# Optimization experiments

Measured on AMD Instinct MI355X. Metric: run time of the kernel, lower is better.

The kernel has to match this reference:

```python
import jax, jax.numpy as jnp
import numpy as np

DIM = 1024
HDS = 16
HEAD_DIM = DIM // HDS
ISC = True


def setup_inputs() -> dict:
    key = jax.random.key(0)
    k = jax.random.split(key, 5)
    x = jax.random.normal(k[0], (4, 2048, DIM), dtype=jnp.float32)
    # Linear(dim, 3*dim): weight [3*dim, dim] (torch layout), bias [3*dim]
    scale = 1.0 / np.sqrt(DIM)
    w_qkv = jax.random.uniform(k[1], (3 * DIM, DIM), jnp.float32, -scale, scale)
    b_qkv = jax.random.uniform(k[2], (3 * DIM,), jnp.float32, -scale, scale)
    w_out = jax.random.uniform(k[3], (DIM, DIM), jnp.float32, -scale, scale)
    b_out = jax.random.uniform(k[4], (DIM,), jnp.float32, -scale, scale)
    return {"x": x, "w_qkv": w_qkv, "b_qkv": b_qkv, "w_out": w_out, "b_out": b_out}


def reference(x, w_qkv, b_qkv, w_out, b_out):
    b, s, dim = x.shape
    # QKV projection: x @ w_qkv.T + b_qkv -> split into q, k, v
    qkv = jnp.einsum('bsd,ed->bse', x, w_qkv) + b_qkv
    q, k, v = jnp.split(qkv, 3, axis=-1)
    # [b, s, dim] -> [b, h, s, hd]
    def to_heads(t):
        return t.reshape(b, s, HDS, HEAD_DIM).transpose(0, 2, 1, 3)
    q, k, v = to_heads(q), to_heads(k), to_heads(v)
    att = jnp.einsum('bhqd,bhkd->bhqk', q, k) * (HEAD_DIM ** -0.5)
    if ISC:
        mask = jnp.triu(jnp.ones((s, s), dtype=bool), k=1)  # True above diagonal
        att = jnp.where(mask[None, None], -jnp.inf, att)
    att = jax.nn.softmax(att, axis=-1)
    # dropout is identity in eval mode
    out = jnp.einsum('bhqk,bhkd->bhqd', att, v)
    out = out.transpose(0, 2, 1, 3).reshape(b, s, dim)
    out = jnp.einsum('bsd,ed->bse', out, w_out) + b_out
    return out
```

## Files before the change

kernel.cpp:

```cpp
#include <hip/hip_runtime.h>
#include <stdint.h>

typedef __bf16 bf16x8 __attribute__((ext_vector_type(8)));
typedef short s16x8 __attribute__((ext_vector_type(8)));
typedef short s16x4 __attribute__((ext_vector_type(4)));
typedef float f32x4 __attribute__((ext_vector_type(4)));
typedef unsigned short u16;

#define K_DIM 1024

static __device__ __forceinline__ u16 f2bf(float f) {
    uint32_t x = __float_as_uint(f);
    x += 0x7fffu + ((x >> 16) & 1u);
    return (u16)(x >> 16);
}

static __device__ __forceinline__ f32x4 mfma16(s16x8 a, s16x8 b, f32x4 c) {
    return __builtin_amdgcn_mfma_f32_16x16x32_bf16(
        __builtin_bit_cast(bf16x8, a), __builtin_bit_cast(bf16x8, b), c, 0, 0, 0);
}

static __device__ __forceinline__ void gload16(const u16* g, u16* l) {
    __builtin_amdgcn_global_load_lds(
        (const __attribute__((address_space(1))) void*)g,
        (__attribute__((address_space(3))) void*)l,
        16, 0, 0);
}

static __device__ __forceinline__ uint32_t cvt_pk_bf16(float lo, float hi) {
    uint32_t r;
    asm("v_cvt_pk_bf16_f32 %0, %1, %2" : "=v"(r) : "v"(lo), "v"(hi));
    return r;
}

static __device__ __forceinline__ float fexp2(float x) {
#if __has_builtin(__builtin_amdgcn_exp2f)
    return __builtin_amdgcn_exp2f(x);
#else
    return __expf(x * 0.69314718056f);
#endif
}

__global__ void cvt_f2bf(const float* __restrict__ in, u16* __restrict__ out, int n4) {
    int stride = gridDim.x * blockDim.x;
    for (int i = blockIdx.x * blockDim.x + threadIdx.x; i < n4; i += stride) {
        float4 f = ((const float4*)in)[i];
        ushort4 o;
        o.x = f2bf(f.x); o.y = f2bf(f.y); o.z = f2bf(f.z); o.w = f2bf(f.w);
        ((ushort4*)out)[i] = o;
    }
}

__global__ __launch_bounds__(256) void gemm_qkv(
    const u16* __restrict__ A, const u16* __restrict__ B,
    const float* __restrict__ bias,
    u16* __restrict__ qo, u16* __restrict__ ko, u16* __restrict__ vto)
{
    __shared__ u16 smem[16384];
    u16* ct = smem;
    const int tid = threadIdx.x;
    const int w = tid >> 6, l = tid & 63;
    const int lr = l & 15, lc = l >> 4;

    const int flat = blockIdx.y * 64 + blockIdx.x;
    const int swz = (flat & 7) * 192 + (flat >> 3);
    const int m0 = (swz & 63) * 128, n0 = (swz >> 6) * 128;
    const int wm = (w >> 1) * 64, wn = (w & 1) * 64;

    const int srow = w * 32 + (l >> 2);
    const int scol = (l & 3) * 8;
    const u16* gA = A + (size_t)(m0 + srow) * K_DIM + scol;
    const u16* gB = B + (size_t)(n0 + srow) * K_DIM + scol;

    f32x4 acc[4][4] = {};

    auto stage = [&](int k0, int buf) {
        u16* lA = smem + buf * 8192 + w * 1024;
        u16* lB = smem + buf * 8192 + 4096 + w * 1024;
        gload16(gA + k0, lA);
        gload16(gA + 16 * K_DIM + k0, lA + 512);
        gload16(gB + k0, lB);
        gload16(gB + 16 * K_DIM + k0, lB + 512);
    };

    stage(0, 0);
    int cur = 0;

    for (int k0 = 0; k0 < K_DIM; k0 += 32) {
        __syncthreads();
        if (k0 + 32 < K_DIM) stage(k0 + 32, cur ^ 1);
        const u16* As = smem + cur * 8192;
        const u16* Bs = As + 4096;
        s16x8 a[4], b[4];
        #pragma unroll
        for (int i = 0; i < 4; ++i)
            a[i] = *(const s16x8*)&As[(wm + i * 16 + lr) * 32 + lc * 8];
        #pragma unroll
        for (int j = 0; j < 4; ++j)
            b[j] = *(const s16x8*)&Bs[(wn + j * 16 + lr) * 32 + lc * 8];
        #pragma unroll
        for (int i = 0; i < 4; ++i)
            #pragma unroll
            for (int j = 0; j < 4; ++j)
                acc[i][j] = mfma16(a[i], b[j], acc[i][j]);
        cur ^= 1;
    }

    const int sec = n0 >> 10;
    const int bb = m0 >> 11, s0 = m0 & 2047;

    if (sec < 2) {
        #pragma unroll
        for (int j = 0; j < 4; ++j) {
            const int n = n0 + wn + j * 16 + lr;
            const float bv = bias[n];
            const int h = (n & 1023) >> 6, d = n & 63;
            #pragma unroll
            for (int i = 0; i < 4; ++i) {
                #pragma unroll
                for (int r = 0; r < 4; ++r) {
                    const int m = m0 + wm + i * 16 + lc * 4 + r;
                    const int s = m & 2047;
                    float v = acc[i][j][r] + bv;
                    if (sec == 0)
                        qo[((size_t)((bb * 16 + h) * 2048 + s)) * 64 + d] = f2bf(v * 0.18033688f);
                    else
                        ko[((size_t)((bb * 16 + h) * 2048 + s)) * 64 + d] = f2bf(v);
                }
            }
        }
    } else {
        __syncthreads();
        #pragma unroll
        for (int jj = 0; jj < 4; ++jj) {
            const int nl = (wn >> 6) * 16 + lr;
            const float bv = bias[n0 + wn + jj * 16 + lr];
            #pragma unroll
            for (int i = 0; i < 4; ++i) {
                const int mloc = wm + i * 16 + lc * 4;
                uint2 pk;
                pk.x = cvt_pk_bf16(acc[i][jj][0] + bv, acc[i][jj][1] + bv);
                pk.y = cvt_pk_bf16(acc[i][jj][2] + bv, acc[i][jj][3] + bv);
                *(s16x4*)&ct[nl * 136 + mloc] = __builtin_bit_cast(s16x4, pk);
            }
            __syncthreads();
            #pragma unroll
            for (int rep = 0; rep < 2; ++rep) {
                const int col = tid >> 3;
                const int seg = (tid & 7) + rep * 8;
                const int nn = n0 + (col >> 4) * 64 + jj * 16 + (col & 15);
                const int h = (nn & 1023) >> 6, d = nn & 63;
                const int mo = seg * 8;
                s16x8 v = *(const s16x8*)&ct[col * 136 + mo];
                *(s16x8*)&vto[((size_t)((bb * 16 + h) * 64 + d)) * 2048 + s0 + mo] = v;
            }
            __syncthreads();
        }
    }
}

__global__ __launch_bounds__(256, 2) void attn_fwd(
    const u16* __restrict__ q, const u16* __restrict__ k,
    const u16* __restrict__ vt, u16* __restrict__ ao)
{
    __shared__ u16 kt[2][8 * 512];
    __shared__ u16 vtl[2][8 * 512];
    __shared__ u16 plds[4 * 32 * 72];
    const int w = threadIdx.x >> 6, l = threadIdx.x & 63;
    const int lr = l & 15, lc = l >> 4;
    const int bh = blockIdx.x;
    const int cp = blockIdx.y;
    const u16* qp = q + (size_t)bh * 2048 * 64;
    const u16* kp = k + (size_t)bh * 2048 * 64;
    const u16* vp = vt + (size_t)bh * 64 * 2048;
    u16* pl = &plds[w * 2304];
    const int bb = bh >> 4, h = bh & 15;

    for (int pass = 0; pass < 2; ++pass) {
        const int C = pass ? (15 - cp) : cp;
        const int q0 = C * 128 + w * 32;
        const int nb = 2 * C + 2;
        const int diag = 2 * C + (w >> 1);

        s16x8 aQ[2][2];
        #pragma unroll
        for (int i = 0; i < 2; ++i)
            #pragma unroll
            for (int kk = 0; kk < 2; ++kk)
                aQ[i][kk] = *(const s16x8*)&qp[(q0 + i * 16 + lr) * 64 + kk * 32 + lc * 8];

        f32x4 O[2][4] = {};
        f32x4 lsv[2] = {};

        auto stage = [&](int t, int buf) {
            const int c0 = t * 64;
            if (w < 2) {
                #pragma unroll
                for (int gi = 0; gi < 4; ++gi) {
                    const int g = w * 4 + gi;
                    const int j = g >> 1, kk = g & 1;
                    gload16(kp + (c0 + j * 16 + lr) * 64 + kk * 32 + lc * 8,
                            &kt[buf][g * 512]);
                }
            } else {
                #pragma unroll
                for (int gi = 0; gi < 4; ++gi) {
                    const int g = (w - 2) * 4 + gi;
                    const int jd = g >> 1, kk = g & 1;
                    gload16(vp + (jd * 16 + lr) * 2048 + c0 + kk * 32 + lc * 8,
                            &vtl[buf][g * 512]);
                }
            }
        };

        __syncthreads();
        stage(0, 0);
        int cur = 0;

        for (int t = 0; t < nb; ++t) {
            __syncthreads();
            if (t + 1 < nb) stage(t + 1, cur ^ 1);

            if (t <= diag) {
                const int c0 = t * 64;
                f32x4 s[2][4] = {};
                __builtin_amdgcn_s_setprio(1);
                #pragma unroll
                for (int j = 0; j < 4; ++j) {
                    s16x8 k0 = *(const s16x8*)&kt[cur][(j * 2 + 0) * 512 + l * 8];
                    s16x8 k1 = *(const s16x8*)&kt[cur][(j * 2 + 1) * 512 + l * 8];
                    s[0][j] = mfma16(k0, aQ[0][0], s[0][j]);
                    s[0][j] = mfma16(k1, aQ[0][1], s[0][j]);
                    s[1][j] = mfma16(k0, aQ[1][0], s[1][j]);
                    s[1][j] = mfma16(k1, aQ[1][1], s[1][j]);
                }
                __builtin_amdgcn_s_setprio(0);
                if (t == diag) {
                    #pragma unroll
                    for (int i = 0; i < 2; ++i) {
                        const int qrow = q0 + i * 16 + lr;
                        #pragma unroll
                        for (int j = 0; j < 4; ++j) {
                            const int kvb = c0 + j * 16 + lc * 4;
                            #pragma unroll
                            for (int r = 0; r < 4; ++r)
                                if (kvb + r > qrow) s[i][j][r] = -1e30f;
                        }
                    }
                }
                #pragma unroll
                for (int i = 0; i < 2; ++i) {
                    #pragma unroll
                    for (int j = 0; j < 4; ++j)
                        #pragma unroll
                        for (int r = 0; r < 4; ++r)
                            s[i][j][r] = fexp2(s[i][j][r]);
                    lsv[i] += (s[i][0] + s[i][1]) + (s[i][2] + s[i][3]);
                    #pragma unroll
                    for (int j = 0; j < 4; ++j) {
                        uint2 pk;
                        pk.x = cvt_pk_bf16(s[i][j][0], s[i][j][1]);
                        pk.y = cvt_pk_bf16(s[i][j][2], s[i][j][3]);
                        *(s16x4*)&pl[(i * 16 + lr) * 72 + j * 16 + lc * 4] =
                            __builtin_bit_cast(s16x4, pk);
                    }
                }
                s16x8 aP[2][2];
                #pragma unroll
                for (int i = 0; i < 2; ++i)
                    #pragma unroll
                    for (int kk = 0; kk < 2; ++kk)
                        aP[i][kk] = *(const s16x8*)&pl[(i * 16 + lr) * 72 + kk * 32 + lc * 8];
                __builtin_amdgcn_s_setprio(1);
                #pragma unroll
                for (int jd = 0; jd < 4; ++jd) {
                    s16x8 v0 = *(const s16x8*)&vtl[cur][(jd * 2 + 0) * 512 + l * 8];
                    s16x8 v1 = *(const s16x8*)&vtl[cur][(jd * 2 + 1) * 512 + l * 8];
                    O[0][jd] = mfma16(aP[0][0], v0, O[0][jd]);
                    O[0][jd] = mfma16(aP[0][1], v1, O[0][jd]);
                    O[1][jd] = mfma16(aP[1][0], v0, O[1][jd]);
                    O[1][jd] = mfma16(aP[1][1], v1, O[1][jd]);
                }
                __builtin_amdgcn_s_setprio(0);
            }
            cur ^= 1;
        }

        float lsr[2];
        #pragma unroll
        for (int i = 0; i < 2; ++i) {
            float t2 = (lsv[i][0] + lsv[i][1]) + (lsv[i][2] + lsv[i][3]);
            t2 += __shfl_xor(t2, 16);
            t2 += __shfl_xor(t2, 32);
            lsr[i] = 1.0f / t2;
        }
        float inv[2][4];
        #pragma unroll
        for (int i = 0; i < 2; ++i)
            #pragma unroll
            for (int r = 0; r < 4; ++r)
                inv[i][r] = __shfl(lsr[i], lc * 4 + r);

        #pragma unroll
        for (int i = 0; i < 2; ++i)
            #pragma unroll
            for (int jd = 0; jd < 4; ++jd)
                #pragma unroll
                for (int r = 0; r < 4; ++r) {
                    const int srow = q0 + i * 16 + lc * 4 + r;
                    ao[((size_t)(bb * 2048 + srow)) * 1024 + h * 64 + jd * 16 + lr] =
                        f2bf(O[i][jd][r] * inv[i][r]);
                }
    }
}

__global__ __launch_bounds__(256) void gemm_out(
    const u16* __restrict__ A, const u16* __restrict__ B,
    const float* __restrict__ bias, float* __restrict__ out)
{
    __shared__ u16 smem[16384];
    const int tid = threadIdx.x;
    const int w = tid >> 6, l = tid & 63;
    const int lr = l & 15, lc = l >> 4;
    const int m0 = blockIdx.x * 128, n0 = blockIdx.y * 128;
    const int wm = (w >> 1) * 64, wn = (w & 1) * 64;

    const int srow = w * 32 + (l >> 2);
    const int scol = (l & 3) * 8;
    const u16* gA = A + (size_t)(m0 + srow) * K_DIM + scol;
    const u16* gB = B + (size_t)(n0 + srow) * K_DIM + scol;

    f32x4 acc[4][4] = {};

    auto stage = [&](int k0, int buf) {
        u16* lA = smem + buf * 8192 + w * 1024;
        u16* lB = smem + buf * 8192 + 4096 + w * 1024;
        gload16(gA + k0, lA);
        gload16(gA + 16 * K_DIM + k0, lA + 512);
        gload16(gB + k0, lB);
        gload16(gB + 16 * K_DIM + k0, lB + 512);
    };

    stage(0, 0);
    int cur = 0;

    for (int k0 = 0; k0 < K_DIM; k0 += 32) {
        __syncthreads();
        if (k0 + 32 < K_DIM) stage(k0 + 32, cur ^ 1);
        const u16* As = smem + cur * 8192;
        const u16* Bs = As + 4096;
        s16x8 a[4], b[4];
        #pragma unroll
        for (int i = 0; i < 4; ++i)
            a[i] = *(const s16x8*)&As[(wm + i * 16 + lr) * 32 + lc * 8];
        #pragma unroll
        for (int j = 0; j < 4; ++j)
            b[j] = *(const s16x8*)&Bs[(wn + j * 16 + lr) * 32 + lc * 8];
        #pragma unroll
        for (int i = 0; i < 4; ++i)
            #pragma unroll
            for (int j = 0; j < 4; ++j)
                acc[i][j] = mfma16(a[i], b[j], acc[i][j]);
        cur ^= 1;
    }

    #pragma unroll
    for (int j = 0; j < 4; ++j) {
        const int n = n0 + wn + j * 16 + lr;
        const float bv = bias[n];
        #pragma unroll
        for (int i = 0; i < 4; ++i) {
            #pragma unroll
            for (int r = 0; r < 4; ++r) {
                const int m = m0 + wm + i * 16 + lc * 4 + r;
                out[(size_t)m * 1024 + n] = acc[i][j][r] + bv;
            }
        }
    }
}

extern "C" void kernel_launch(void* const* d_in, const int* in_sizes, int n_in,
                              void* d_out, int out_size, void* d_ws, size_t ws_size,
                              hipStream_t stream) {
    const float* x     = (const float*)d_in[0];
    const float* w_qkv = (const float*)d_in[1];
    const float* b_qkv = (const float*)d_in[2];
    const float* w_out = (const float*)d_in[3];
    const float* b_out = (const float*)d_in[4];
    float* out = (float*)d_out;

    char* ws = (char*)d_ws;
    u16* xb   = (u16*)(ws);
    u16* wqb  = (u16*)(ws + 16777216);
    u16* wob  = (u16*)(ws + 23068672);
    u16* qws  = (u16*)(ws + 25165824);
    u16* kws  = (u16*)(ws + 41943040);
    u16* vtws = (u16*)(ws + 58720256);
    u16* attn = (u16*)(ws + 75497472);

    cvt_f2bf<<<dim3(2048), 256, 0, stream>>>(x,     xb,  8388608 / 4);
    cvt_f2bf<<<dim3(2048), 256, 0, stream>>>(w_qkv, wqb, 3145728 / 4);
    cvt_f2bf<<<dim3(1024), 256, 0, stream>>>(w_out, wob, 1048576 / 4);

    gemm_qkv<<<dim3(64, 24), 256, 0, stream>>>(xb, wqb, b_qkv, qws, kws, vtws);
    attn_fwd<<<dim3(64, 8), 256, 0, stream>>>(qws, kws, vtws, attn);
    gemm_out<<<dim3(64, 8), 256, 0, stream>>>(attn, wob, b_out, out);
}
```

Before: 155.8 us.

## Double GEMM K-tile to 64 and XOR-swizzle LDS layout in projection GEMMs

Both projection GEMMs (QKV and output) now stage 64-wide K tiles instead of 32-wide, which halves the number of barrier-separated iterations. They also store the tiles in LDS with an XOR swizzle on 16-byte chunks, applied consistently on the global-to-LDS load and the fragment reads, to avoid bank conflicts. Shared memory per block doubles to 64 KB, which may reduce how many blocks fit on a CU.

```diff
diff --git a/kernel.cpp b/kernel.cpp
--- a/kernel.cpp
+++ b/kernel.cpp
@@ -56,7 +56,7 @@
     const float* __restrict__ bias,
     u16* __restrict__ qo, u16* __restrict__ ko, u16* __restrict__ vto)
 {
-    __shared__ u16 smem[16384];
+    __shared__ u16 smem[32768];
     u16* ct = smem;
     const int tid = threadIdx.x;
     const int w = tid >> 6, l = tid & 63;
@@ -67,42 +67,49 @@
     const int m0 = (swz & 63) * 128, n0 = (swz >> 6) * 128;
     const int wm = (w >> 1) * 64, wn = (w & 1) * 64;
 
-    const int srow = w * 32 + (l >> 2);
-    const int scol = (l & 3) * 8;
+    const int srow = w * 8 + (l >> 3);
+    const int scol = ((l & 7) ^ (l >> 3)) * 8;
     const u16* gA = A + (size_t)(m0 + srow) * K_DIM + scol;
     const u16* gB = B + (size_t)(n0 + srow) * K_DIM + scol;
 
     f32x4 acc[4][4] = {};
 
     auto stage = [&](int k0, int buf) {
-        u16* lA = smem + buf * 8192 + w * 1024;
-        u16* lB = smem + buf * 8192 + 4096 + w * 1024;
-        gload16(gA + k0, lA);
-        gload16(gA + 16 * K_DIM + k0, lA + 512);
-        gload16(gB + k0, lB);
-        gload16(gB + 16 * K_DIM + k0, lB + 512);
+        u16* base = smem + buf * 16384;
+        #pragma unroll
+        for (int g = 0; g < 4; ++g) {
+            gload16(gA + (size_t)g * 32 * K_DIM + k0, base + (g * 32 + w * 8) * 64);
+            gload16(gB + (size_t)g * 32 * K_DIM + k0, base + 8192 + (g * 32 + w * 8) * 64);
+        }
     };
 
     stage(0, 0);
     int cur = 0;
 
-    for (int k0 = 0; k0 < K_DIM; k0 += 32) {
+    for (int k0 = 0; k0 < K_DIM; k0 += 64) {
         __syncthreads();
-        if (k0 + 32 < K_DIM) stage(k0 + 32, cur ^ 1);
-        const u16* As = smem + cur * 8192;
-        const u16* Bs = As + 4096;
-        s16x8 a[4], b[4];
-        #pragma unroll
-        for (int i = 0; i < 4; ++i)
-            a[i] = *(const s16x8*)&As[(wm + i * 16 + lr) * 32 + lc * 8];
-        #pragma unroll
-        for (int j = 0; j < 4; ++j)
-            b[j] = *(const s16x8*)&Bs[(wn + j * 16 + lr) * 32 + lc * 8];
-        #pragma unroll
-        for (int i = 0; i < 4; ++i)
-            #pragma unroll
-            for (int j = 0; j < 4; ++j)
-                acc[i][j] = mfma16(a[i], b[j], acc[i][j]);
+        if (k0 + 64 < K_DIM) stage(k0 + 64, cur ^ 1);
+        const u16* As = smem + cur * 16384;
+        const u16* Bs = As + 8192;
+        #pragma unroll
+        for (int kk = 0; kk < 2; ++kk) {
+            s16x8 a[4], b[4];
+            #pragma unroll
+            for (int i = 0; i < 4; ++i) {
+                const int row = wm + i * 16 + lr;
+                a[i] = *(const s16x8*)&As[row * 64 + ((kk * 32 + lc * 8) ^ ((row & 7) * 8))];
+            }
+            #pragma unroll
+            for (int j = 0; j < 4; ++j) {
+                const int row = wn + j * 16 + lr;
+                b[j] = *(const s16x8*)&Bs[row * 64 + ((kk * 32 + lc * 8) ^ ((row & 7) * 8))];
+            }
+            #pragma unroll
+            for (int i = 0; i < 4; ++i)
+                #pragma unroll
+                for (int j = 0; j < 4; ++j)
+                    acc[i][j] = mfma16(a[i], b[j], acc[i][j]);
+        }
         cur ^= 1;
     }
 
@@ -318,49 +325,56 @@
     const u16* __restrict__ A, const u16* __restrict__ B,
     const float* __restrict__ bias, float* __restrict__ out)
 {
-    __shared__ u16 smem[16384];
+    __shared__ u16 smem[32768];
     const int tid = threadIdx.x;
     const int w = tid >> 6, l = tid & 63;
     const int lr = l & 15, lc = l >> 4;
     const int m0 = blockIdx.x * 128, n0 = blockIdx.y * 128;
     const int wm = (w >> 1) * 64, wn = (w & 1) * 64;
 
-    const int srow = w * 32 + (l >> 2);
-    const int scol = (l & 3) * 8;
+    const int srow = w * 8 + (l >> 3);
+    const int scol = ((l & 7) ^ (l >> 3)) * 8;
     const u16* gA = A + (size_t)(m0 + srow) * K_DIM + scol;
     const u16* gB = B + (size_t)(n0 + srow) * K_DIM + scol;
 
     f32x4 acc[4][4] = {};
 
     auto stage = [&](int k0, int buf) {
-        u16* lA = smem + buf * 8192 + w * 1024;
-        u16* lB = smem + buf * 8192 + 4096 + w * 1024;
-        gload16(gA + k0, lA);
-        gload16(gA + 16 * K_DIM + k0, lA + 512);
-        gload16(gB + k0, lB);
-        gload16(gB + 16 * K_DIM + k0, lB + 512);
+        u16* base = smem + buf * 16384;
+        #pragma unroll
+        for (int g = 0; g < 4; ++g) {
+            gload16(gA + (size_t)g * 32 * K_DIM + k0, base + (g * 32 + w * 8) * 64);
+            gload16(gB + (size_t)g * 32 * K_DIM + k0, base + 8192 + (g * 32 + w * 8) * 64);
+        }
     };
 
     stage(0, 0);
     int cur = 0;
 
-    for (int k0 = 0; k0 < K_DIM; k0 += 32) {
+    for (int k0 = 0; k0 < K_DIM; k0 += 64) {
         __syncthreads();
-        if (k0 + 32 < K_DIM) stage(k0 + 32, cur ^ 1);
-        const u16* As = smem + cur * 8192;
-        const u16* Bs = As + 4096;
-        s16x8 a[4], b[4];
-        #pragma unroll
-        for (int i = 0; i < 4; ++i)
-            a[i] = *(const s16x8*)&As[(wm + i * 16 + lr) * 32 + lc * 8];
-        #pragma unroll
-        for (int j = 0; j < 4; ++j)
-            b[j] = *(const s16x8*)&Bs[(wn + j * 16 + lr) * 32 + lc * 8];
-        #pragma unroll
-        for (int i = 0; i < 4; ++i)
-            #pragma unroll
-            for (int j = 0; j < 4; ++j)
-                acc[i][j] = mfma16(a[i], b[j], acc[i][j]);
+        if (k0 + 64 < K_DIM) stage(k0 + 64, cur ^ 1);
+        const u16* As = smem + cur * 16384;
+        const u16* Bs = As + 8192;
+        #pragma unroll
+        for (int kk = 0; kk < 2; ++kk) {
+            s16x8 a[4], b[4];
+            #pragma unroll
+            for (int i = 0; i < 4; ++i) {
+                const int row = wm + i * 16 + lr;
+                a[i] = *(const s16x8*)&As[row * 64 + ((kk * 32 + lc * 8) ^ ((row & 7) * 8))];
+            }
+            #pragma unroll
+            for (int j = 0; j < 4; ++j) {
+                const int row = wn + j * 16 + lr;
+                b[j] = *(const s16x8*)&Bs[row * 64 + ((kk * 32 + lc * 8) ^ ((row & 7) * 8))];
+            }
+            #pragma unroll
+            for (int i = 0; i < 4; ++i)
+                #pragma unroll
+                for (int j = 0; j < 4; ++j)
+                    acc[i][j] = mfma16(a[i], b[j], acc[i][j]);
+        }
         cur ^= 1;
     }
 
```

Result: no change. 154.2 us (-1.0%).
